# Kernel optimization log

Hardware: AMD Instinct MI355X
Metric: run time of the kernel (lower is better)

The kernel has to match this reference:

```python
import jax, jax.numpy as jnp
import numpy as np

HID = 512
EMB = 345
SEQ = 512


def _lstm_dir(x, Wih, Whh, b, reverse):
    # x: (S, in), Wih: (4H, in), Whh: (4H, H), b: (4H,)  [torch gate order i,f,g,o]
    H = Whh.shape[1]
    zin = x @ Wih.T + b  # precompute input contribution: (S, 4H)

    def step(carry, z):
        h, c = carry
        z = z + h @ Whh.T
        i, f, g, o = jnp.split(z, 4)
        c = jax.nn.sigmoid(f) * c + jax.nn.sigmoid(i) * jnp.tanh(g)
        h = jax.nn.sigmoid(o) * jnp.tanh(c)
        return (h, c), h

    init = (jnp.zeros((H,), x.dtype), jnp.zeros((H,), x.dtype))
    _, hs = jax.lax.scan(step, init, zin, reverse=reverse)
    return hs  # (S, H), time-aligned for both directions


def _bilstm(x, Wih0, Whh0, b0, Wih_r, Whh_r, b_r):
    out = jnp.concatenate([
        _lstm_dir(x, Wih0[0], Whh0[0], b0[0], False),
        _lstm_dir(x, Wih0[1], Whh0[1], b0[1], True)], axis=-1)
    for l in range(Wih_r.shape[0]):  # remaining 3 stacked layers
        out = jnp.concatenate([
            _lstm_dir(out, Wih_r[l, 0], Whh_r[l, 0], b_r[l, 0], False),
            _lstm_dir(out, Wih_r[l, 1], Whh_r[l, 1], b_r[l, 1], True)], axis=-1)
    return out  # (S, 2H)


def setup_inputs() -> dict:
    key = jax.random.key(0)
    ks = jax.random.split(key, 16)
    H4, H2 = 4 * HID, 2 * HID
    s = 0.05
    x = jax.random.normal(ks[0], (SEQ, EMB), jnp.float32)
    heads = jax.random.randint(ks[1], (SEQ + 1,), 0, SEQ + 1)
    heads = heads.at[0].set(-1)  # root has no head
    Wih0 = jax.random.normal(ks[2], (2, H4, EMB), jnp.float32) * s
    Whh0 = jax.random.normal(ks[3], (2, H4, HID), jnp.float32) * s
    b0 = jax.random.normal(ks[4], (2, H4), jnp.float32) * s
    Wih_r = jax.random.normal(ks[5], (3, 2, H4, H2), jnp.float32) * s
    Whh_r = jax.random.normal(ks[6], (3, 2, H4, HID), jnp.float32) * s
    b_r = jax.random.normal(ks[7], (3, 2, H4), jnp.float32) * s
    W1 = jax.random.normal(ks[8], (256, 2 * H2), jnp.float32) * s
    b1 = jax.random.normal(ks[9], (256,), jnp.float32) * s
    W2 = jax.random.normal(ks[10], (128, 256), jnp.float32) * s
    b2 = jax.random.normal(ks[11], (128,), jnp.float32) * s
    W3 = jax.random.normal(ks[12], (64, 128), jnp.float32) * s
    b3 = jax.random.normal(ks[13], (64,), jnp.float32) * s
    W4 = jax.random.normal(ks[14], (1, 64), jnp.float32) * s
    b4 = jax.random.normal(ks[15], (1,), jnp.float32) * s
    return dict(x=x, heads=heads, Wih0=Wih0, Whh0=Whh0, b0=b0,
                Wih_r=Wih_r, Whh_r=Whh_r, b_r=b_r,
                W1=W1, b1=b1, W2=W2, b2=b2, W3=W3, b3=b3, W4=W4, b4=b4)


def reference(x, heads, Wih0, Whh0, b0, Wih_r, Whh_r, b_r,
              W1, b1, W2, b2, W3, b3, W4, b4):
    lstm_out = _bilstm(x, Wih0, Whh0, b0, Wih_r, Whh_r, b_r)  # (S, 2H)
    H2 = lstm_out.shape[-1]
    avail = jnp.concatenate([jnp.zeros((1, H2), x.dtype), lstm_out], axis=0)  # (N, 2H)
    N = avail.shape[0]
    # network(cat(w1, w2)) split: W1 acts on the two halves independently
    A = avail @ W1[:, :H2].T  # (N, 256)
    B = avail @ W1[:, H2:].T  # (N, 256)
    h1 = jax.nn.relu(A[:, None, :] + B[None, :, :] + b1)  # (N, N, 256)
    h2 = jax.nn.relu(h1 @ W2.T + b2)                       # (N, N, 128)
    h3 = jax.nn.relu(h2 @ W3.T + b3)                       # (N, N, 64)
    S = (h3 @ W4.T + b4)[..., 0]                           # (N, N) raw scores
    T = jnp.where(jnp.arange(N)[None, :] == heads[:, None], 100.0, 0.0)
    loss = jnp.sum((S - T) ** 2) / (N * N)  # sum of per-pair MSE / N^2
    probs = jax.nn.softmax(S, axis=1)  # scipy softmax(score_matrix, axis=1)
    return loss, probs
```

## Files before the change

### kernel.cpp

```cpp
#include <hip/hip_runtime.h>
#include <math.h>

#define HID 512
#define SEQ 512
#define EMB 345
#define NN  513
#define MPAD 576
#define H4  2048
#define H2  1024

__global__ __launch_bounds__(256)
void gemm_nt(const float* __restrict__ A, int lda, long aStride,
             const float* __restrict__ B, int ldb, long bStride,
             const float* __restrict__ bias, long biasStride,
             float* __restrict__ C, int ldc, long cStride, int K)
{
    int z = blockIdx.z;
    A += (long)z * aStride; B += (long)z * bStride; C += (long)z * cStride;
    const float* bptr = bias ? bias + (long)z * biasStride : nullptr;
    __shared__ float As[16][68];
    __shared__ float Bs[16][68];
    int tid = threadIdx.x;
    int tx = tid & 15, ty = tid >> 4;
    int m0 = blockIdx.y * 64, n0 = blockIdx.x * 64;
    float acc[4][4] = {};
    for (int k0 = 0; k0 < K; k0 += 16) {
        #pragma unroll
        for (int i = 0; i < 4; i++) {
            int id = tid + 256 * i;
            int mn = id >> 4, kk = id & 15;
            int k = k0 + kk;
            As[kk][mn] = (k < K) ? A[(long)(m0 + mn) * lda + k] : 0.f;
            Bs[kk][mn] = (k < K) ? B[(long)(n0 + mn) * ldb + k] : 0.f;
        }
        __syncthreads();
        #pragma unroll
        for (int kk = 0; kk < 16; kk++) {
            float a[4], b[4];
            #pragma unroll
            for (int i = 0; i < 4; i++) a[i] = As[kk][ty * 4 + i];
            #pragma unroll
            for (int j = 0; j < 4; j++) b[j] = Bs[kk][tx * 4 + j];
            #pragma unroll
            for (int i = 0; i < 4; i++)
                #pragma unroll
                for (int j = 0; j < 4; j++) acc[i][j] += a[i] * b[j];
        }
        __syncthreads();
    }
    #pragma unroll
    for (int i = 0; i < 4; i++) {
        int m = m0 + ty * 4 + i;
        #pragma unroll
        for (int j = 0; j < 4; j++) {
            int n = n0 + tx * 4 + j;
            float v = acc[i][j];
            if (bptr) v += bptr[n];
            C[(long)m * ldc + n] = v;
        }
    }
}

__device__ __forceinline__ float sigmf(float x)
{ return __builtin_amdgcn_rcpf(1.f + __expf(-x)); }
__device__ __forceinline__ float tanhf_fast(float x)
{ return 1.f - 2.f * __builtin_amdgcn_rcpf(1.f + __expf(2.f * x)); }

__device__ __forceinline__ bool badw(unsigned long long a)
{ return ((unsigned)a == 0xFFFFFFFFu) || ((unsigned)(a >> 32) == 0xFFFFFFFFu); }

__global__ __launch_bounds__(256, 1)
void lstm_layer(const float* __restrict__ zin,
                const float* __restrict__ Whh,
                float* out)
{
    int wg  = blockIdx.x;
    int dir = wg >> 6;
    int cb  = (wg & 63) * 8;
    int tid = threadIdx.x;
    int ci  = tid >> 5;
    int g   = (tid >> 3) & 3;
    int kp  = tid & 7;
    int cell = cb + ci;
    long row = (long)g * 512 + cell;

    __shared__ float w_lds[64 * 256];
    __shared__ float h_st[2][8 * 68];

    {
        const float4* wp = (const float4*)(Whh + ((long)dir * H4 + row) * HID + kp * 64);
        #pragma unroll
        for (int j4 = 0; j4 < 16; j4++) {
            float4 w = wp[j4];
            w_lds[(4 * j4 + 0) * 256 + tid] = w.x;
            w_lds[(4 * j4 + 1) * 256 + tid] = w.y;
            w_lds[(4 * j4 + 2) * 256 + tid] = w.z;
            w_lds[(4 * j4 + 3) * 256 + tid] = w.w;
        }
    }

    const float* zin_d = zin + (long)dir * SEQ * H4;
    float c_st = 0.f;
    bool actlane = ((tid & 31) == 0);
    int hc = tid >> 5;
    int ho = 2 * (tid & 31);

    for (int t = 0; t < SEQ; t++) {
        int at = (dir == 0) ? t : (SEQ - 1 - t);
        float wv[64];
        #pragma unroll
        for (int j = 0; j < 64; j++) wv[j] = w_lds[j * 256 + tid];
        float zv = 0.f;
        if (kp == 0) zv = zin_d[(long)at * H4 + (long)g * 512 + cell];

        if (t == 0) {
            *(float2*)&h_st[0][hc * 68 + ho] = make_float2(0.f, 0.f);
        } else {
            int at_prev = (dir == 0) ? (t - 1) : (SEQ - t);
            const unsigned long long* src =
                (const unsigned long long*)(out + (long)at_prev * H2 + dir * HID) + tid;
            unsigned long long a = __hip_atomic_load(src, __ATOMIC_RELAXED, __HIP_MEMORY_SCOPE_AGENT);
            while (badw(a)) {
                __builtin_amdgcn_s_sleep(1);
                a = __hip_atomic_load(src, __ATOMIC_RELAXED, __HIP_MEMORY_SCOPE_AGENT);
            }
            union { unsigned long long u; float2 f; } cv; cv.u = a;
            *(float2*)&h_st[t & 1][hc * 68 + ho] = cv.f;
        }
        __syncthreads();

        const float4* hp = (const float4*)&h_st[t & 1][kp * 68];
        float acc = 0.f;
        #pragma unroll
        for (int j4 = 0; j4 < 16; j4++) {
            float4 h = hp[j4];
            acc += wv[4*j4+0] * h.x + wv[4*j4+1] * h.y
                 + wv[4*j4+2] * h.z + wv[4*j4+3] * h.w;
        }
        acc += __shfl_xor(acc, 1);
        acc += __shfl_xor(acc, 2);
        acc += __shfl_xor(acc, 4);
        float zsum = acc + zv;
        float zf = __shfl(zsum, (tid & 32) + 8);
        float zg = __shfl(zsum, (tid & 32) + 16);
        float zo = __shfl(zsum, (tid & 32) + 24);
        if (actlane) {
            float cc = sigmf(zf) * c_st + sigmf(zsum) * tanhf_fast(zg);
            c_st = cc;
            float hh = sigmf(zo) * tanhf_fast(cc);
            __hip_atomic_store(out + (long)at * H2 + dir * HID + cell, hh,
                               __ATOMIC_RELAXED, __HIP_MEMORY_SCOPE_AGENT);
        }
    }
}

__global__ __launch_bounds__(256)
void build_avail(const float* __restrict__ lstm_out, float* __restrict__ avail)
{
    long idx = (long)blockIdx.x * 256 + threadIdx.x;
    if (idx >= (long)MPAD * H2) return;
    int i = (int)(idx >> 10);
    int c = (int)(idx & 1023);
    float v = 0.f;
    if (i >= 1 && i <= SEQ) v = lstm_out[(long)(i - 1) * H2 + c];
    avail[idx] = v;
}

__global__ __launch_bounds__(256)
void transpose_w(const float* __restrict__ W, float* __restrict__ WT, int rows, int cols)
{
    int idx = blockIdx.x * 256 + threadIdx.x;
    if (idx >= rows * cols) return;
    int rr = idx / cols, cc = idx % cols;
    WT[cc * rows + rr] = W[idx];
}

#define STR1 257
#define STR2 129
__global__ __launch_bounds__(256)
void pair_kernel(const float* __restrict__ Abuf, const float* __restrict__ Bbuf,
                 const float* __restrict__ b1, const float* __restrict__ W2T,
                 const float* __restrict__ b2, const float* __restrict__ W3T,
                 const float* __restrict__ b3, const float* __restrict__ W4,
                 const float* __restrict__ b4, float* __restrict__ S)
{
    __shared__ float At[8 * STR1];
    __shared__ float Bt[8 * STR1];
    __shared__ float b1s[256];
    __shared__ float h2s[64 * STR2];
    __shared__ float spart[4 * 64];
    int tid = threadIdx.x;
    int i0 = blockIdx.y * 8, j0 = blockIdx.x * 8;
    {
        int rr = tid >> 5;
        int cbase = (tid & 31) * 8;
        #pragma unroll
        for (int u = 0; u < 8; u++) {
            At[rr * STR1 + cbase + u] = Abuf[(long)(i0 + rr) * 256 + cbase + u];
            Bt[rr * STR1 + cbase + u] = Bbuf[(long)(j0 + rr) * 256 + cbase + u];
        }
        b1s[tid] = b1[tid];
    }
    __syncthreads();
    int w = tid >> 6;
    int lane = tid & 63;
    int ii = lane >> 3, jj = lane & 7;
    #pragma unroll 1
    for (int blk = 0; blk < 4; blk++) {
        int c2b = __builtin_amdgcn_readfirstlane(w * 32 + blk * 8);
        float acc[8] = {};
        #pragma unroll 4
        for (int c1 = 0; c1 < 256; c1++) {
            float h1v = At[ii * STR1 + c1] + Bt[jj * STR1 + c1] + b1s[c1];
            h1v = fmaxf(h1v, 0.f);
            const float* wrow = W2T + c1 * 128 + c2b;
            #pragma unroll
            for (int u = 0; u < 8; u++) acc[u] += wrow[u] * h1v;
        }
        #pragma unroll
        for (int u = 0; u < 8; u++)
            h2s[lane * STR2 + c2b + u] = fmaxf(acc[u] + b2[c2b + u], 0.f);
    }
    __syncthreads();
    float sp = 0.f;
    #pragma unroll 1
    for (int blk = 0; blk < 2; blk++) {
        int c3b = __builtin_amdgcn_readfirstlane(w * 16 + blk * 8);
        float acc[8] = {};
        #pragma unroll 4
        for (int c2 = 0; c2 < 128; c2++) {
            float h2v = h2s[lane * STR2 + c2];
            const float* wrow = W3T + c2 * 64 + c3b;
            #pragma unroll
            for (int u = 0; u < 8; u++) acc[u] += wrow[u] * h2v;
        }
        #pragma unroll
        for (int u = 0; u < 8; u++) {
            float v = fmaxf(acc[u] + b3[c3b + u], 0.f);
            sp += W4[c3b + u] * v;
        }
    }
    spart[w * 64 + lane] = sp;
    __syncthreads();
    if (tid < 64) {
        float s = spart[tid] + spart[64 + tid] + spart[128 + tid] + spart[192 + tid] + b4[0];
        int i = i0 + (tid >> 3), j = j0 + (tid & 7);
        if (i < NN && j < NN) S[(long)i * NN + j] = s;
    }
}

__global__ __launch_bounds__(256)
void softmax_row(const float* __restrict__ S, const int* __restrict__ heads,
                 float* __restrict__ probs, float* __restrict__ rowloss)
{
    int i = blockIdx.x;
    int tid = threadIdx.x;
    __shared__ float red[256];
    __shared__ float srow[NN];
    const float* Si = S + (long)i * NN;
    float mx = -1e30f;
    for (int j = tid; j < NN; j += 256) { float v = Si[j]; srow[j] = v; mx = fmaxf(mx, v); }
    red[tid] = mx; __syncthreads();
    for (int s = 128; s > 0; s >>= 1) { if (tid < s) red[tid] = fmaxf(red[tid], red[tid + s]); __syncthreads(); }
    mx = red[0]; __syncthreads();
    float sum = 0.f, sq = 0.f;
    int hd = heads[i];
    for (int j = tid; j < NN; j += 256) {
        float v = srow[j];
        sum += __expf(v - mx);
        float t = (j == hd) ? 100.f : 0.f;
        float d = v - t; sq += d * d;
    }
    red[tid] = sum; __syncthreads();
    for (int s = 128; s > 0; s >>= 1) { if (tid < s) red[tid] += red[tid + s]; __syncthreads(); }
    sum = red[0]; __syncthreads();
    red[tid] = sq; __syncthreads();
    for (int s = 128; s > 0; s >>= 1) { if (tid < s) red[tid] += red[tid + s]; __syncthreads(); }
    if (tid == 0) rowloss[i] = red[0];
    float inv = 1.f / sum;
    for (int j = tid; j < NN; j += 256) probs[(long)i * NN + j] = __expf(srow[j] - mx) * inv;
}

__global__ __launch_bounds__(256)
void finish_loss(const float* __restrict__ rowloss, float* __restrict__ out0)
{
    __shared__ float red[256];
    int tid = threadIdx.x;
    float s = 0.f;
    for (int i = tid; i < NN; i += 256) s += rowloss[i];
    red[tid] = s; __syncthreads();
    for (int k = 128; k > 0; k >>= 1) { if (tid < k) red[tid] += red[tid + k]; __syncthreads(); }
    if (tid == 0) out0[0] = red[0] / ((float)NN * (float)NN);
}

extern "C" void kernel_launch(void* const* d_in, const int* in_sizes, int n_in,
                              void* d_out, int out_size, void* d_ws, size_t ws_size,
                              hipStream_t stream)
{
    const float* x     = (const float*)d_in[0];
    const int*   heads = (const int*)  d_in[1];
    const float* Wih0  = (const float*)d_in[2];
    const float* Whh0  = (const float*)d_in[3];
    const float* b0    = (const float*)d_in[4];
    const float* Wih_r = (const float*)d_in[5];
    const float* Whh_r = (const float*)d_in[6];
    const float* b_r   = (const float*)d_in[7];
    const float* W1    = (const float*)d_in[8];
    const float* b1    = (const float*)d_in[9];
    const float* W2    = (const float*)d_in[10];
    const float* b2    = (const float*)d_in[11];
    const float* W3    = (const float*)d_in[12];
    const float* b3    = (const float*)d_in[13];
    const float* W4    = (const float*)d_in[14];
    const float* b4    = (const float*)d_in[15];
    float* out = (float*)d_out;

    char* ws = (char*)d_ws;
    const size_t o_zin  = 0;
    const size_t o_outA = o_zin  + (size_t)2 * SEQ * H4 * 4 + 512;
    const size_t o_outB = o_outA + (size_t)SEQ * H2 * 4 + 512;
    const size_t o_avail= o_outB + (size_t)SEQ * H2 * 4 + 512;
    const size_t o_Abuf = o_avail+ (size_t)MPAD * H2 * 4 + 512;
    const size_t o_Bbuf = o_Abuf + (size_t)MPAD * 256 * 4 + 512;
    const size_t o_W2T  = o_Bbuf + (size_t)MPAD * 256 * 4 + 512;
    const size_t o_W3T  = o_W2T  + 256 * 128 * 4 + 512;
    const size_t o_S    = o_W3T  + 128 * 64 * 4 + 512;
    const size_t o_rl   = o_S    + (size_t)NN * NN * 4 + 512;

    float* zin   = (float*)(ws + o_zin);
    float* outA  = (float*)(ws + o_outA);
    float* outB  = (float*)(ws + o_outB);
    float* avail = (float*)(ws + o_avail);
    float* Abuf  = (float*)(ws + o_Abuf);
    float* Bbuf  = (float*)(ws + o_Bbuf);
    float* W2T   = (float*)(ws + o_W2T);
    float* W3T   = (float*)(ws + o_W3T);
    float* Sbuf  = (float*)(ws + o_S);
    float* rowl  = (float*)(ws + o_rl);

    const size_t outBytes = (size_t)SEQ * H2 * 4;

    gemm_nt<<<dim3(H4 / 64, SEQ / 64, 2), 256, 0, stream>>>(
        x, EMB, 0, Wih0, EMB, (long)H4 * EMB, b0, H4,
        zin, H4, (long)SEQ * H4, EMB);
    hipMemsetAsync(outA, 0xFF, outBytes, stream);
    lstm_layer<<<128, 256, 0, stream>>>(zin, Whh0, outA);

    float* bufs[2] = { outA, outB };
    for (int l = 1; l <= 3; l++) {
        const float* src = bufs[(l - 1) & 1];
        float* dst = bufs[l & 1];
        gemm_nt<<<dim3(H4 / 64, SEQ / 64, 2), 256, 0, stream>>>(
            src, H2, 0, Wih_r + (size_t)(l - 1) * 2 * H4 * H2, H2, (long)H4 * H2,
            b_r + (size_t)(l - 1) * 2 * H4, H4,
            zin, H4, (long)SEQ * H4, H2);
        hipMemsetAsync(dst, 0xFF, outBytes, stream);
        lstm_layer<<<128, 256, 0, stream>>>(
            zin, Whh_r + (size_t)(l - 1) * 2 * H4 * HID, dst);
    }
    float* lstm_final = bufs[3 & 1];

    build_avail<<<(MPAD * H2) / 256, 256, 0, stream>>>(lstm_final, avail);

    gemm_nt<<<dim3(256 / 64, MPAD / 64, 1), 256, 0, stream>>>(
        avail, H2, 0, W1, 2048, 0, nullptr, 0, Abuf, 256, 0, H2);
    gemm_nt<<<dim3(256 / 64, MPAD / 64, 1), 256, 0, stream>>>(
        avail, H2, 0, W1 + 1024, 2048, 0, nullptr, 0, Bbuf, 256, 0, H2);

    transpose_w<<<(128 * 256) / 256, 256, 0, stream>>>(W2, W2T, 128, 256);
    transpose_w<<<(64 * 128) / 256, 256, 0, stream>>>(W3, W3T, 64, 128);

    pair_kernel<<<dim3(65, 65), 256, 0, stream>>>(
        Abuf, Bbuf, b1, W2T, b2, W3T, b3, W4, b4, Sbuf);

    softmax_row<<<NN, 256, 0, stream>>>(Sbuf, heads, out + 1, rowl);
    finish_loss<<<1, 256, 0, stream>>>(rowl, out);
}
```

Before: 5.094 ms.

## Keep LSTM recurrent weights in registers across 256 workgroups

The persistent LSTM layer kernel now runs 256 workgroups instead of 128, each owning 4 cells with one wavefront per cell. Each thread holds 32 recurrent weights in registers for the whole sequence, which removes the per-timestep reload of 64 weights from LDS and the 64 KB LDS weight buffer. The dot product is split 16 ways per gate, so the shuffle reduction gains one extra level, and more workgroups must spin-wait on the global h handoff each step. This relies on all 256 workgroups being co-resident on the device for the cross-workgroup polling to make progress.

```diff
diff --git a/kernel.cpp b/kernel.cpp
--- a/kernel.cpp
+++ b/kernel.cpp
@@ -75,46 +75,37 @@
                 float* out)
 {
     int wg  = blockIdx.x;
-    int dir = wg >> 6;
-    int cb  = (wg & 63) * 8;
-    int tid = threadIdx.x;
-    int ci  = tid >> 5;
-    int g   = (tid >> 3) & 3;
-    int kp  = tid & 7;
-    int cell = cb + ci;
+    int dir = wg >> 7;
+    int cb  = (wg & 127) * 4;
+    int tid = threadIdx.x;
+    int w   = tid >> 6;
+    int l   = tid & 63;
+    int g   = l >> 4;
+    int kp  = l & 15;
+    int cell = cb + w;
     long row = (long)g * 512 + cell;
 
-    __shared__ float w_lds[64 * 256];
-    __shared__ float h_st[2][8 * 68];
-
+    __shared__ float h_st[2][16 * 36];
+
+    float4 wv[8];
     {
-        const float4* wp = (const float4*)(Whh + ((long)dir * H4 + row) * HID + kp * 64);
-        #pragma unroll
-        for (int j4 = 0; j4 < 16; j4++) {
-            float4 w = wp[j4];
-            w_lds[(4 * j4 + 0) * 256 + tid] = w.x;
-            w_lds[(4 * j4 + 1) * 256 + tid] = w.y;
-            w_lds[(4 * j4 + 2) * 256 + tid] = w.z;
-            w_lds[(4 * j4 + 3) * 256 + tid] = w.w;
-        }
+        const float4* wp = (const float4*)(Whh + ((long)dir * H4 + row) * HID + kp * 32);
+        #pragma unroll
+        for (int j = 0; j < 8; j++) wv[j] = wp[j];
     }
 
     const float* zin_d = zin + (long)dir * SEQ * H4;
     float c_st = 0.f;
-    bool actlane = ((tid & 31) == 0);
-    int hc = tid >> 5;
-    int ho = 2 * (tid & 31);
+    int hc = tid >> 4;
+    int ho = 2 * (tid & 15);
 
     for (int t = 0; t < SEQ; t++) {
         int at = (dir == 0) ? t : (SEQ - 1 - t);
-        float wv[64];
-        #pragma unroll
-        for (int j = 0; j < 64; j++) wv[j] = w_lds[j * 256 + tid];
         float zv = 0.f;
-        if (kp == 0) zv = zin_d[(long)at * H4 + (long)g * 512 + cell];
+        if (kp == 0) zv = zin_d[(long)at * H4 + row];
 
         if (t == 0) {
-            *(float2*)&h_st[0][hc * 68 + ho] = make_float2(0.f, 0.f);
+            *(float2*)&h_st[0][hc * 36 + ho] = make_float2(0.f, 0.f);
         } else {
             int at_prev = (dir == 0) ? (t - 1) : (SEQ - t);
             const unsigned long long* src =
@@ -125,26 +116,26 @@
                 a = __hip_atomic_load(src, __ATOMIC_RELAXED, __HIP_MEMORY_SCOPE_AGENT);
             }
             union { unsigned long long u; float2 f; } cv; cv.u = a;
-            *(float2*)&h_st[t & 1][hc * 68 + ho] = cv.f;
+            *(float2*)&h_st[t & 1][hc * 36 + ho] = cv.f;
         }
         __syncthreads();
 
-        const float4* hp = (const float4*)&h_st[t & 1][kp * 68];
+        const float4* hp = (const float4*)&h_st[t & 1][kp * 36];
         float acc = 0.f;
         #pragma unroll
-        for (int j4 = 0; j4 < 16; j4++) {
-            float4 h = hp[j4];
-            acc += wv[4*j4+0] * h.x + wv[4*j4+1] * h.y
-                 + wv[4*j4+2] * h.z + wv[4*j4+3] * h.w;
+        for (int j = 0; j < 8; j++) {
+            float4 h = hp[j];
+            acc += wv[j].x * h.x + wv[j].y * h.y + wv[j].z * h.z + wv[j].w * h.w;
         }
         acc += __shfl_xor(acc, 1);
         acc += __shfl_xor(acc, 2);
         acc += __shfl_xor(acc, 4);
+        acc += __shfl_xor(acc, 8);
         float zsum = acc + zv;
-        float zf = __shfl(zsum, (tid & 32) + 8);
-        float zg = __shfl(zsum, (tid & 32) + 16);
-        float zo = __shfl(zsum, (tid & 32) + 24);
-        if (actlane) {
+        float zf = __shfl(zsum, 16);
+        float zg = __shfl(zsum, 32);
+        float zo = __shfl(zsum, 48);
+        if (l == 0) {
             float cc = sigmf(zf) * c_st + sigmf(zsum) * tanhf_fast(zg);
             c_st = cc;
             float hh = sigmf(zo) * tanhf_fast(cc);
@@ -344,7 +335,7 @@
         x, EMB, 0, Wih0, EMB, (long)H4 * EMB, b0, H4,
         zin, H4, (long)SEQ * H4, EMB);
     hipMemsetAsync(outA, 0xFF, outBytes, stream);
-    lstm_layer<<<128, 256, 0, stream>>>(zin, Whh0, outA);
+    lstm_layer<<<256, 256, 0, stream>>>(zin, Whh0, outA);
 
     float* bufs[2] = { outA, outB };
     for (int l = 1; l <= 3; l++) {
@@ -355,7 +346,7 @@
             b_r + (size_t)(l - 1) * 2 * H4, H4,
             zin, H4, (long)SEQ * H4, H2);
         hipMemsetAsync(dst, 0xFF, outBytes, stream);
-        lstm_layer<<<128, 256, 0, stream>>>(
+        lstm_layer<<<256, 256, 0, stream>>>(
             zin, Whh_r + (size_t)(l - 1) * 2 * H4 * HID, dst);
     }
     float* lstm_final = bufs[3 & 1];
```

After: 8.425 ms. +65.4%, slower.
